# Performance work log

Measured on AMD Instinct MI355X. Metric: run time of the kernel, lower is better.

The kernel has to match this reference:

```python
import jax, jax.numpy as jnp
import numpy as np

IN_DIM, HID, OUT = 256, 10, 50
LEN_S = 4096
GAUSSIAN_DEGREE = 1


def _pdist2(a, b):
    # squared pairwise L2 distance, clamped at 0
    an = jnp.sum(a * a, axis=1)[:, None]
    bn = jnp.sum(b * b, axis=1)[None, :]
    d = an + bn - 2.0 * (a @ b.T)
    return jnp.maximum(d, 0.0)


def _mlp(x, W1, b1, W2, b2, W3, b3, W4, b4):
    h = jax.nn.softplus(x @ W1 + b1)
    h = jax.nn.softplus(h @ W2 + b2)
    h = jax.nn.softplus(h @ W3 + b3)
    return h @ W4 + b4


def setup_inputs() -> dict:
    key = jax.random.key(0)
    ks = jax.random.split(key, 12)
    inp = {
        "X": jax.random.normal(ks[0], (LEN_S, IN_DIM), jnp.float32),
        "Y": jax.random.normal(ks[1], (LEN_S, IN_DIM), jnp.float32),
        "W1": jax.random.normal(ks[2], (IN_DIM, HID), jnp.float32) / np.sqrt(IN_DIM),
        "b1": jnp.zeros((HID,), jnp.float32),
        "W2": jax.random.normal(ks[3], (HID, HID), jnp.float32) / np.sqrt(HID),
        "b2": jnp.zeros((HID,), jnp.float32),
        "W3": jax.random.normal(ks[4], (HID, HID), jnp.float32) / np.sqrt(HID),
        "b3": jnp.zeros((HID,), jnp.float32),
        "W4": jax.random.normal(ks[5], (HID, OUT), jnp.float32) / np.sqrt(HID),
        "b4": jnp.zeros((OUT,), jnp.float32),
        "epsilon_opt": jnp.array(np.log(5e-11), jnp.float32),
        "sigma_q_opt": jnp.array(np.sqrt(2 * 32 * 32), jnp.float32),
        "sigma_phi_opt": jnp.array(np.sqrt(0.005), jnp.float32),
    }
    return inp


def _deep_mmd(X, Y, W1, b1, W2, b2, W3, b3, W4, b4, epsilon_opt, sigma_q_opt, sigma_phi_opt):
    feats_org = jnp.concatenate([X, Y], axis=0)
    feats = _mlp(feats_org, W1, b1, W2, b2, W3, b3, W4, b4)
    epsilon = jax.nn.sigmoid(epsilon_opt)
    sigma_q = sigma_q_opt ** 2
    sigma_phi = sigma_phi_opt ** 2

    nx = ny = LEN_S
    x, y = feats[:nx], feats[nx:]
    xo, yo = feats_org[:nx], feats_org[nx:]

    def kernel(a, b, ao, bo):
        d = _pdist2(a, b)
        do = _pdist2(ao, bo)
        smooth = jnp.exp(-((d / sigma_phi) ** GAUSSIAN_DEGREE) - do / sigma_q)
        return (1.0 - epsilon) * smooth + epsilon * jnp.exp(-do / sigma_q)

    k_x = kernel(x, x, xo, xo)
    k_y = kernel(y, y, yo, yo)
    k_xy = kernel(x, y, xo, yo)

    # unbiased MMD estimate
    xx = (jnp.sum(k_x) - jnp.trace(k_x)) / (nx * (nx - 1))
    yy = (jnp.sum(k_y) - jnp.trace(k_y)) / (ny * (ny - 1))
    xy = (jnp.sum(k_xy) - jnp.trace(k_xy)) / (nx * (ny - 1))
    mmd2 = xx - 2.0 * xy + yy

    # variance estimate
    h = k_x + k_y - k_xy - k_xy.T
    hs = jnp.sum(h, axis=1)
    v1 = (4.0 / ny ** 3) * jnp.dot(hs, hs)
    v2 = (4.0 / nx ** 4) * jnp.sum(h) ** 2
    var = v1 - v2 + 1e-8
    return jnp.stack([mmd2, var])


def reference(X, Y, W1, b1, W2, b2, W3, b3, W4, b4, epsilon_opt, sigma_q_opt, sigma_phi_opt):
    return _deep_mmd(X, Y, W1, b1, W2, b2, W3, b3, W4, b4, epsilon_opt, sigma_q_opt, sigma_phi_opt)
```

## Files before the change

### kernel.cpp

```cpp
#include <hip/hip_runtime.h>
#include <math.h>


#define N_S 4096
#define LOG2E 1.4426950408889634

typedef _Float16 v8h __attribute__((ext_vector_type(8)));
typedef float v16f __attribute__((ext_vector_type(16)));

union U16 { uint4 u; v8h h; };

__device__ __forceinline__ void pack_hilo(const float* fv, uint4* hi, uint4* lo) {
    U16 H, L;
#pragma unroll
    for (int u = 0; u < 8; ++u) {
        _Float16 h = (_Float16)fv[u];
        H.h[u] = h;
        L.h[u] = (_Float16)(fv[u] - (float)h);
    }
    *hi = H.u; *lo = L.u;
}

__device__ __forceinline__ uint4 pack_hi(const float* fv) {
    U16 H;
#pragma unroll
    for (int u = 0; u < 8; ++u) H.h[u] = (_Float16)fv[u];
    return H.u;
}

__device__ __forceinline__ void gload16(const void* g, void* lds) {
    __builtin_amdgcn_global_load_lds(
        (const __attribute__((address_space(1))) unsigned int*)g,
        (__attribute__((address_space(3))) unsigned int*)lds, 16, 0, 0);
}

__global__ __launch_bounds__(256)
void mlp_kernel(const float* __restrict__ X, const float* __restrict__ Y,
                const float* __restrict__ W1, const float* __restrict__ b1,
                const float* __restrict__ W2, const float* __restrict__ b2,
                const float* __restrict__ W3, const float* __restrict__ b3,
                const float* __restrict__ W4, const float* __restrict__ b4,
                const float* __restrict__ sq,
                uint4* __restrict__ PK, float* __restrict__ normF,
                float* __restrict__ wOrg,
                float* __restrict__ D8, double* __restrict__ S)
{
    __shared__ double sW1[8 * 330];
    __shared__ double sW2[100], sW3[100], sW4[500];
    __shared__ double sb1[10], sb2[10], sb3[10], sb4[50];
    int tid = threadIdx.x;
    int gt = blockIdx.x * 256 + tid;

    if (gt < 8192) D8[gt] = 0.0f;
    else if (gt < 8196) S[gt - 8192] = 0.0;

    {
        int kg = tid >> 5, kl = tid & 31;
#pragma unroll
        for (int j = 0; j < 10; ++j)
            sW1[kg * 330 + kl * 10 + j] = (double)W1[tid * 10 + j];
    }
    for (int i = tid; i < 100; i += 256) { sW2[i] = (double)W2[i]; sW3[i] = (double)W3[i]; }
    for (int i = tid; i < 500; i += 256) sW4[i] = (double)W4[i];
    if (tid < 10) { sb1[tid] = (double)b1[tid]; sb2[tid] = (double)b2[tid]; sb3[tid] = (double)b3[tid]; }
    if (tid < 50) sb4[tid] = (double)b4[tid];
    __syncthreads();

    int r = gt >> 3, g = gt & 7;
    const float* xr = (r < N_S) ? (X + (size_t)r * 256) : (Y + (size_t)(r - N_S) * 256);
    const float* xrg = xr + g * 32;
    const double* w1g = sW1 + g * 330;

    float xl[32];
    double z[10];
#pragma unroll
    for (int j = 0; j < 10; ++j) z[j] = 0.0;
    double nrm = 0.0;
    for (int k4 = 0; k4 < 32; k4 += 4) {
        float4 xv4 = *(const float4*)(xrg + k4);
        xl[k4] = xv4.x; xl[k4 + 1] = xv4.y; xl[k4 + 2] = xv4.z; xl[k4 + 3] = xv4.w;
        double xv[4] = {(double)xv4.x, (double)xv4.y, (double)xv4.z, (double)xv4.w};
#pragma unroll
        for (int u = 0; u < 4; ++u) {
            nrm += xv[u] * xv[u];
#pragma unroll
            for (int j = 0; j < 10; ++j) z[j] += xv[u] * w1g[(k4 + u) * 10 + j];
        }
    }
    {
        size_t base = (size_t)r * 48 + g * 4;
#pragma unroll
        for (int u = 0; u < 4; ++u)
            PK[base + u] = pack_hi(&xl[u * 8]);
    }

#pragma unroll
    for (int off = 1; off < 8; off <<= 1) {
        nrm += __shfl_xor(nrm, off);
#pragma unroll
        for (int j = 0; j < 10; ++j) z[j] += __shfl_xor(z[j], off);
    }
#pragma unroll
    for (int j = 0; j < 10; ++j) z[j] += sb1[j];
#pragma unroll
    for (int j = 0; j < 10; ++j) z[j] = fmax(z[j], 0.0) + log1p(exp(-fabs(z[j])));

    double z2[10];
#pragma unroll
    for (int j = 0; j < 10; ++j) z2[j] = sb2[j];
#pragma unroll
    for (int k = 0; k < 10; ++k)
#pragma unroll
        for (int j = 0; j < 10; ++j) z2[j] += z[k] * sW2[k * 10 + j];
#pragma unroll
    for (int j = 0; j < 10; ++j) z2[j] = fmax(z2[j], 0.0) + log1p(exp(-fabs(z2[j])));

    double z3[10];
#pragma unroll
    for (int j = 0; j < 10; ++j) z3[j] = sb3[j];
#pragma unroll
    for (int k = 0; k < 10; ++k)
#pragma unroll
        for (int j = 0; j < 10; ++j) z3[j] += z2[k] * sW3[k * 10 + j];
#pragma unroll
    for (int j = 0; j < 10; ++j) z3[j] = fmax(z3[j], 0.0) + log1p(exp(-fabs(z3[j])));

    double nf = 0.0;
    float ff[8];
#pragma unroll
    for (int u = 0; u < 8; ++u) ff[u] = 0.0f;
#pragma unroll
    for (int j = 0; j < 50; ++j) {
        double f = sb4[j];
#pragma unroll
        for (int k = 0; k < 10; ++k) f += z3[k] * sW4[k * 50 + j];
        nf += f * f;
        if ((j >> 3) == g) ff[j & 7] = (float)f;
    }
    {
        uint4 hi, lo;
        pack_hilo(ff, &hi, &lo);
        size_t fb = (size_t)r * 48 + 32 + (g >> 2) * 8 + (g & 3);
        PK[fb] = hi;
        PK[fb + 4] = lo;
    }

    if (g == 0) {
        double sqv = (double)sq[0];
        double co = LOG2E / (sqv * sqv);
        wOrg[r] = (float)exp2(-nrm * co);
    }
    if (g == 1) normF[r] = (float)nf;
}

__device__ __forceinline__ v8h ldfrag8(const uint4* buf, int s, int g) {
    U16 t; t.u = buf[s * 8 + (g ^ (s & 7))];
    return t.h;
}
__device__ __forceinline__ v8h ldfrag4(const uint4* buf, int s, int g) {
    U16 t; t.u = buf[s * 4 + (g ^ (s & 3))];
    return t.h;
}

__global__ __launch_bounds__(512, 4)
void pair_kernel(const uint4* __restrict__ PK, const float* __restrict__ normF,
                 const float* __restrict__ wOrg,
                 const float* __restrict__ ep, const float* __restrict__ sq,
                 const float* __restrict__ sph,
                 float* __restrict__ D8, double* __restrict__ S)
{
    __shared__ __align__(16) char smem[65536];

    int tid = threadIdx.x;
    int lane = tid & 63, w = tid >> 6;
    int wr2 = w >> 2, wc4 = w & 3;

    int orig = blockIdx.x;
    int L = (orig & 7) * 260 + (orig >> 3);
    int it = (int)((129.0 - sqrt(16641.0 - 8.0 * (double)L)) * 0.5);
    while (it * (129 - it) / 2 > L) --it;
    while ((it + 1) * (128 - it) / 2 <= L) ++it;
    int jt = it + (L - it * (129 - it) / 2);
    int i0 = it * 128, j0 = jt * 128;

    auto stage = [&](int t, int hb) {
        char* Ab = smem + hb * 32768;
        if (t < 8) {
            char* Bb = Ab + 8192;
            int rr = tid >> 2, slot = tid & 3, hg = slot ^ (rr & 3);
            const uint4* ga = &PK[(size_t)(i0 + rr) * 48 + t * 4 + hg];
            const uint4* gb = &PK[(size_t)(j0 + rr) * 48 + t * 4 + hg];
            char* la = Ab + (w << 10);
            char* lb = Bb + (w << 10);
            gload16(ga, la);
            gload16(gb, lb);
        } else {
            char* Bb = Ab + 16384;
#pragma unroll
            for (int i = 0; i < 2; ++i) {
                int u = i * 512 + tid;
                int rr = u >> 3, hg = (u & 7) ^ (rr & 7);
                const uint4* ga = &PK[(size_t)(i0 + rr) * 48 + 32 + (t - 8) * 8 + hg];
                const uint4* gb = &PK[(size_t)(j0 + rr) * 48 + 32 + (t - 8) * 8 + hg];
                char* la = Ab + (i * 512 + (w << 6)) * 16;
                char* lb = Bb + (i * 512 + (w << 6)) * 16;
                gload16(ga, la);
                gload16(gb, lb);
            }
        }
    };

    stage(0, 0);

    bool sameHalf = (jt < 32) || (it >= 32);
    bool isDiag = (it == jt);
    bool isTrace = (jt == it + 32);
    int region = (jt < 32) ? 0 : ((it >= 32) ? 1 : 2);
    float sgn = sameHalf ? 1.0f : -1.0f;

    int rs0 = wr2 * 64 + (lane & 31), rs1 = rs0 + 32;
    int cs = wc4 * 32 + (lane & 31);

    auto mfma_org = [&](int hb, v16f& a0, v16f& a1) {
        const uint4* Ab = (const uint4*)(smem + hb * 32768);
        const uint4* Bb = (const uint4*)(smem + hb * 32768 + 8192);
#pragma unroll
        for (int ks = 0; ks < 2; ++ks) {
            int gl = ks * 2 + (lane >> 5);
            v8h ah0 = ldfrag4(Ab, rs0, gl), ah1 = ldfrag4(Ab, rs1, gl);
            v8h bh = ldfrag4(Bb, cs, gl);
            a0 = __builtin_amdgcn_mfma_f32_32x32x16_f16(ah0, bh, a0, 0, 0, 0);
            a1 = __builtin_amdgcn_mfma_f32_32x32x16_f16(ah1, bh, a1, 0, 0, 0);
        }
    };
    auto mfma_feat = [&](int hb, v16f& a0, v16f& a1) {
        const uint4* Ab = (const uint4*)(smem + hb * 32768);
        const uint4* Bb = (const uint4*)(smem + hb * 32768 + 16384);
#pragma unroll
        for (int ks = 0; ks < 2; ++ks) {
            int gl = ks * 2 + (lane >> 5);
            v8h ah0 = ldfrag8(Ab, rs0, gl), ah1 = ldfrag8(Ab, rs1, gl);
            v8h al0 = ldfrag8(Ab, rs0, 4 + gl), al1 = ldfrag8(Ab, rs1, 4 + gl);
            v8h bh = ldfrag8(Bb, cs, gl), bl = ldfrag8(Bb, cs, 4 + gl);
            a0 = __builtin_amdgcn_mfma_f32_32x32x16_f16(al0, bh, a0, 0, 0, 0);
            a0 = __builtin_amdgcn_mfma_f32_32x32x16_f16(ah0, bl, a0, 0, 0, 0);
            a0 = __builtin_amdgcn_mfma_f32_32x32x16_f16(ah0, bh, a0, 0, 0, 0);
            a1 = __builtin_amdgcn_mfma_f32_32x32x16_f16(al1, bh, a1, 0, 0, 0);
            a1 = __builtin_amdgcn_mfma_f32_32x32x16_f16(ah1, bl, a1, 0, 0, 0);
            a1 = __builtin_amdgcn_mfma_f32_32x32x16_f16(ah1, bh, a1, 0, 0, 0);
        }
    };

    v16f accG0{}, accG1{}, accF0{}, accF1{};

#pragma unroll
    for (int t = 0; t < 10; ++t) {
        int hb = t & 1;
        asm volatile("s_waitcnt vmcnt(0)" ::: "memory");
        __builtin_amdgcn_sched_barrier(0);
        __builtin_amdgcn_s_barrier();
        __builtin_amdgcn_sched_barrier(0);
        if (t < 9) stage(t + 1, hb ^ 1);
        __builtin_amdgcn_s_setprio(1);
        if (t < 8) mfma_org(hb, accG0, accG1);
        else       mfma_feat(hb, accF0, accF1);
        __builtin_amdgcn_s_setprio(0);
    }
    __syncthreads();

    double epd = (double)ep[0];
    double eps = 1.0 / (1.0 + exp(-epd));
    double sqv = (double)sq[0], spv = (double)sph[0];
    float cf = (float)(LOG2E / (spv * spv));
    float twoco = (float)(2.0 * LOG2E / (sqv * sqv));
    float epsv = (float)eps, ome = (float)(1.0 - eps);

    float* E2 = (float*)smem;

    double bsum = 0.0, trsum = 0.0;
    float colacc = 0.0f;
    int cl = wc4 * 32 + (lane & 31);
    float wb = wOrg[j0 + cl];
    float nbF = normF[j0 + cl];

    auto evalacc = [&](const v16f& aG, const v16f& aF, int rbase) {
        float4 wa4[4], na4[4];
#pragma unroll
        for (int q = 0; q < 4; ++q) {
            int rb = i0 + rbase + 4 * (lane >> 5) + 8 * q;
            wa4[q] = *(const float4*)&wOrg[rb];
            na4[q] = *(const float4*)&normF[rb];
        }
#pragma unroll
        for (int reg = 0; reg < 16; ++reg) {
            int rl = rbase + 4 * (lane >> 5) + (reg & 3) + 8 * (reg >> 2);
            float wa = ((const float*)&wa4[reg >> 2])[reg & 3];
            float naA = ((const float*)&na4[reg >> 2])[reg & 3];
            float dfeat = fmaxf(naA + nbF - 2.0f * aF[reg], 0.0f);
            float e2v = exp2f(-dfeat * cf);
            float kv = wa * wb * exp2f(aG[reg] * twoco) * (ome * e2v + epsv);
            if (isDiag && rl == cl) kv = 0.0f;
            if (isTrace && cl == rl) trsum += (double)kv;
            bsum += (double)kv;
            colacc += kv;
            E2[rl * 128 + cl] = kv;
        }
    };
    evalacc(accG0, accF0, wr2 * 64);
    evalacc(accG1, accF1, wr2 * 64 + 32);
    __syncthreads();

    {
        int row = tid >> 2, q = tid & 3;
        float s = 0.0f;
#pragma unroll
        for (int c = 0; c < 8; ++c) {
            int cc = (c + row) & 7;
            float4 v = *(const float4*)&E2[row * 128 + q * 32 + cc * 4];
            s += v.x + v.y + v.z + v.w;
        }
        s += __shfl_xor(s, 1);
        s += __shfl_xor(s, 2);
        if (q == 0) atomicAdd(&D8[i0 + row], sgn * s);
    }

    if (!isDiag) {
        atomicAdd(&D8[j0 + cl], sgn * colacc);
    }

#pragma unroll
    for (int off = 32; off > 0; off >>= 1) bsum += __shfl_down(bsum, off);
    if (isTrace) {
#pragma unroll
        for (int off = 32; off > 0; off >>= 1) trsum += __shfl_down(trsum, off);
    }
    __syncthreads();
    double* dred = (double*)smem;
    if (lane == 0) { dred[w] = bsum; dred[8 + w] = trsum; }
    __syncthreads();
    if (tid == 0) {
        double wgt = (sameHalf && !isDiag) ? 2.0 : 1.0;
        double t0 = 0.0, t1 = 0.0;
#pragma unroll
        for (int q = 0; q < 8; ++q) { t0 += dred[q]; t1 += dred[8 + q]; }
        atomicAdd(&S[region], wgt * t0);
        if (isTrace) atomicAdd(&S[3], t1);
    }
}

__global__ __launch_bounds__(256)
void final_kernel(const float* __restrict__ D8, const double* __restrict__ S,
                  float* __restrict__ out)
{
    __shared__ double buf[512];
    int tid = threadIdx.x;
    double sD = 0, sD2 = 0;
    for (int i = tid; i < 4096; i += 256) {
        double d = (double)D8[i] + (double)D8[i + 4096];
        sD += d; sD2 += d * d;
    }
    buf[tid] = sD; buf[256 + tid] = sD2;
    __syncthreads();
    for (int s = 128; s > 0; s >>= 1) {
        if (tid < s) { buf[tid] += buf[tid + s]; buf[256 + tid] += buf[256 + tid + s]; }
        __syncthreads();
    }
    if (tid == 0) {
        double n = (double)N_S, D = n * (n - 1.0);
        double xx = S[0] / D, yy = S[1] / D, xy = (S[2] - S[3]) / D;
        double mmd2 = xx - 2.0 * xy + yy;
        double sumd = buf[0], sumd2 = buf[256];
        double sumh = 2.0 * n + sumd;
        double sumhs2 = 4.0 * n + 4.0 * sumd + sumd2;
        double n3 = n * n * n, n4 = n3 * n;
        double var = 4.0 / n3 * sumhs2 - 4.0 / n4 * sumh * sumh + 1e-8;
        out[0] = (float)mmd2;
        out[1] = (float)var;
    }
}

extern "C" void kernel_launch(void* const* d_in, const int* in_sizes, int n_in,
                              void* d_out, int out_size, void* d_ws, size_t ws_size,
                              hipStream_t stream)
{
    const float* X   = (const float*)d_in[0];
    const float* Y   = (const float*)d_in[1];
    const float* W1  = (const float*)d_in[2];
    const float* b1  = (const float*)d_in[3];
    const float* W2  = (const float*)d_in[4];
    const float* b2  = (const float*)d_in[5];
    const float* W3  = (const float*)d_in[6];
    const float* b3  = (const float*)d_in[7];
    const float* W4  = (const float*)d_in[8];
    const float* b4  = (const float*)d_in[9];
    const float* ep  = (const float*)d_in[10];
    const float* sq  = (const float*)d_in[11];
    const float* sph = (const float*)d_in[12];
    float* out = (float*)d_out;

    char* ws = (char*)d_ws;
    uint4*  PK    = (uint4*)ws;
    float*  wOrg  = (float*)(ws + 6291456);
    float*  normF = (float*)(ws + 6324224);
    float*  D8    = (float*)(ws + 6356992);
    double* S     = (double*)(ws + 6389760);

    mlp_kernel<<<256, 256, 0, stream>>>(X, Y, W1, b1, W2, b2, W3, b3, W4, b4,
                                        sq, PK, normF, wOrg, D8, S);

    pair_kernel<<<2080, 512, 0, stream>>>(PK, normF, wOrg, ep, sq, sph, D8, S);

    final_kernel<<<1, 256, 0, stream>>>(D8, S, out);
}
```

Before: 186.0 us.

## Use k-major shared-memory layout and merge original-feature stages into fewer larger ones

Shared memory is restaged as a k-slot-major layout (slot*128+row) so fragment loads index without an XOR swizzle. The original-feature K loop is merged from 8 stages of 4 slots into 4 stages of 8 slots, which cuts the pipeline to 6 barrier-separated stages. The row-reduction read rotation is also changed to spread LDS banks. Fewer syncs and simpler addressing are the aim, at the risk of bank conflicts in the new layout and larger per-stage loads.

```diff
diff --git a/kernel.cpp b/kernel.cpp
--- a/kernel.cpp
+++ b/kernel.cpp
@@ -153,12 +153,8 @@
     if (g == 1) normF[r] = (float)nf;
 }
 
-__device__ __forceinline__ v8h ldfrag8(const uint4* buf, int s, int g) {
-    U16 t; t.u = buf[s * 8 + (g ^ (s & 7))];
-    return t.h;
-}
-__device__ __forceinline__ v8h ldfrag4(const uint4* buf, int s, int g) {
-    U16 t; t.u = buf[s * 4 + (g ^ (s & 3))];
+__device__ __forceinline__ v8h ldsm(const uint4* buf, int s, int g) {
+    U16 t; t.u = buf[g * 128 + s];
     return t.h;
 }
 
@@ -185,28 +181,18 @@
 
     auto stage = [&](int t, int hb) {
         char* Ab = smem + hb * 32768;
-        if (t < 8) {
-            char* Bb = Ab + 8192;
-            int rr = tid >> 2, slot = tid & 3, hg = slot ^ (rr & 3);
-            const uint4* ga = &PK[(size_t)(i0 + rr) * 48 + t * 4 + hg];
-            const uint4* gb = &PK[(size_t)(j0 + rr) * 48 + t * 4 + hg];
-            char* la = Ab + (w << 10);
-            char* lb = Bb + (w << 10);
+        char* Bb = Ab + 16384;
+        int soff = (t < 4) ? t * 8 : 32 + (t - 4) * 8;
+#pragma unroll
+        for (int i = 0; i < 2; ++i) {
+            int u = i * 512 + tid;
+            int row = u & 127, s8 = u >> 7;
+            const uint4* ga = &PK[(size_t)(i0 + row) * 48 + soff + s8];
+            const uint4* gb = &PK[(size_t)(j0 + row) * 48 + soff + s8];
+            char* la = Ab + (i * 512 + (w << 6)) * 16;
+            char* lb = Bb + (i * 512 + (w << 6)) * 16;
             gload16(ga, la);
             gload16(gb, lb);
-        } else {
-            char* Bb = Ab + 16384;
-#pragma unroll
-            for (int i = 0; i < 2; ++i) {
-                int u = i * 512 + tid;
-                int rr = u >> 3, hg = (u & 7) ^ (rr & 7);
-                const uint4* ga = &PK[(size_t)(i0 + rr) * 48 + 32 + (t - 8) * 8 + hg];
-                const uint4* gb = &PK[(size_t)(j0 + rr) * 48 + 32 + (t - 8) * 8 + hg];
-                char* la = Ab + (i * 512 + (w << 6)) * 16;
-                char* lb = Bb + (i * 512 + (w << 6)) * 16;
-                gload16(ga, la);
-                gload16(gb, lb);
-            }
         }
     };
 
@@ -223,12 +209,12 @@
 
     auto mfma_org = [&](int hb, v16f& a0, v16f& a1) {
         const uint4* Ab = (const uint4*)(smem + hb * 32768);
-        const uint4* Bb = (const uint4*)(smem + hb * 32768 + 8192);
-#pragma unroll
-        for (int ks = 0; ks < 2; ++ks) {
+        const uint4* Bb = (const uint4*)(smem + hb * 32768 + 16384);
+#pragma unroll
+        for (int ks = 0; ks < 4; ++ks) {
             int gl = ks * 2 + (lane >> 5);
-            v8h ah0 = ldfrag4(Ab, rs0, gl), ah1 = ldfrag4(Ab, rs1, gl);
-            v8h bh = ldfrag4(Bb, cs, gl);
+            v8h ah0 = ldsm(Ab, rs0, gl), ah1 = ldsm(Ab, rs1, gl);
+            v8h bh = ldsm(Bb, cs, gl);
             a0 = __builtin_amdgcn_mfma_f32_32x32x16_f16(ah0, bh, a0, 0, 0, 0);
             a1 = __builtin_amdgcn_mfma_f32_32x32x16_f16(ah1, bh, a1, 0, 0, 0);
         }
@@ -239,9 +225,9 @@
 #pragma unroll
         for (int ks = 0; ks < 2; ++ks) {
             int gl = ks * 2 + (lane >> 5);
-            v8h ah0 = ldfrag8(Ab, rs0, gl), ah1 = ldfrag8(Ab, rs1, gl);
-            v8h al0 = ldfrag8(Ab, rs0, 4 + gl), al1 = ldfrag8(Ab, rs1, 4 + gl);
-            v8h bh = ldfrag8(Bb, cs, gl), bl = ldfrag8(Bb, cs, 4 + gl);
+            v8h ah0 = ldsm(Ab, rs0, gl), ah1 = ldsm(Ab, rs1, gl);
+            v8h al0 = ldsm(Ab, rs0, 4 + gl), al1 = ldsm(Ab, rs1, 4 + gl);
+            v8h bh = ldsm(Bb, cs, gl), bl = ldsm(Bb, cs, 4 + gl);
             a0 = __builtin_amdgcn_mfma_f32_32x32x16_f16(al0, bh, a0, 0, 0, 0);
             a0 = __builtin_amdgcn_mfma_f32_32x32x16_f16(ah0, bl, a0, 0, 0, 0);
             a0 = __builtin_amdgcn_mfma_f32_32x32x16_f16(ah0, bh, a0, 0, 0, 0);
@@ -254,15 +240,15 @@
     v16f accG0{}, accG1{}, accF0{}, accF1{};
 
 #pragma unroll
-    for (int t = 0; t < 10; ++t) {
+    for (int t = 0; t < 6; ++t) {
         int hb = t & 1;
         asm volatile("s_waitcnt vmcnt(0)" ::: "memory");
         __builtin_amdgcn_sched_barrier(0);
         __builtin_amdgcn_s_barrier();
         __builtin_amdgcn_sched_barrier(0);
-        if (t < 9) stage(t + 1, hb ^ 1);
+        if (t < 5) stage(t + 1, hb ^ 1);
         __builtin_amdgcn_s_setprio(1);
-        if (t < 8) mfma_org(hb, accG0, accG1);
+        if (t < 4) mfma_org(hb, accG0, accG1);
         else       mfma_feat(hb, accF0, accF1);
         __builtin_amdgcn_s_setprio(0);
     }
@@ -312,10 +298,11 @@
 
     {
         int row = tid >> 2, q = tid & 3;
+        int rot = ((q << 1) | (row & 1));
         float s = 0.0f;
 #pragma unroll
         for (int c = 0; c < 8; ++c) {
-            int cc = (c + row) & 7;
+            int cc = (c + rot) & 7;
             float4 v = *(const float4*)&E2[row * 128 + q * 32 + cc * 4];
             s += v.x + v.y + v.z + v.w;
         }
```

Result: slower. 194.9 us (+4.8%).
